# Kernel tuning notes

Hardware: AMD Instinct MI355X
Metric: run time of the kernel (lower is better)

The kernel has to match this reference:

```python
import jax, jax.numpy as jnp
import numpy as np

KROT = 8        # number of pairwise-rotation layers (hard-coded in Rotation)
GROUP = 128     # rotation group size (hard-coded)
QGS = 128       # quantization group size (hard-coded in RotateLinearAWQMarlinInt4)


def setup_inputs() -> dict:
    rng = np.random.default_rng(0)
    M, K, N = 32, 8192, 28672
    G = K // QGS  # 64 quant groups
    shifts = np.arange(8, dtype=np.uint32) * 4
    # activations
    x = jnp.asarray(rng.standard_normal((M, K)), dtype=jnp.float16)
    # int4 weights packed 8-per-int32 along the out dim (nibble j of word n -> column n*8+j)
    nib = rng.integers(0, 16, size=(K, N // 8, 8), dtype=np.uint32)
    qweight = jnp.asarray((nib << shifts).sum(-1, dtype=np.uint32).view(np.int32))  # (K, N//8)
    znib = rng.integers(0, 16, size=(G, N // 8, 8), dtype=np.uint32)
    qzeros = jnp.asarray((znib << shifts).sum(-1, dtype=np.uint32).view(np.int32))  # (G, N//8)
    scales = jnp.asarray(rng.uniform(0.001, 0.01, (G, N)), dtype=jnp.float16)
    bias = jnp.asarray(rng.standard_normal(N) * 0.01, dtype=jnp.float16)
    # rotation params: per-layer angles over all K//2 pairs; one local permutation of
    # 0..127 per layer, shared across all K//GROUP groups (as in Rotation.__init__)
    theta = jnp.asarray(rng.uniform(-0.2, 0.2, (KROT, K // 2)), dtype=jnp.float16)
    pairs = jnp.asarray(np.stack([rng.permutation(GROUP) for _ in range(KROT)]).astype(np.int32))  # (KROT, 128)
    channel_scales = jnp.asarray(rng.uniform(0.5, 2.0, (1, K)), dtype=jnp.float16)
    return dict(x=x, qweight=qweight, qzeros=qzeros, scales=scales, bias=bias,
                theta=theta, pairs=pairs, channel_scales=channel_scales)


def _rotate(x, pairs, theta, channel_scales):
    # x: (M, K). Apply KROT layers of Givens rotations on channel pairs within each
    # 128-wide group, then per-channel scaling.
    M, K = x.shape
    ng = K // GROUP
    xg = x.reshape(M, ng, GROUP)
    for k in range(KROT):
        p = pairs[k]                      # (128,) local permutation
        i, j = p[0::2], p[1::2]           # (64,) disjoint index sets
        th = theta[k].reshape(ng, GROUP // 2).astype(jnp.float32)  # (ng, 64) per-group angles
        c = jnp.cos(th).astype(x.dtype)
        s = jnp.sin(th).astype(x.dtype)
        xi = xg[:, :, i]
        xj = xg[:, :, j]
        xg = xg.at[:, :, i].set(c * xi - s * xj)
        xg = xg.at[:, :, j].set(s * xi + c * xj)
    return xg.reshape(M, K) * channel_scales


def _dequant(qweight, qzeros, scales):
    # unpack 8 uint4 nibbles per int32 along the out dim; dequant per quant group
    K = qweight.shape[0]
    shifts = jnp.arange(8, dtype=jnp.int32) * 4
    w = ((qweight[:, :, None] >> shifts) & 0xF).reshape(K, -1)       # (K, N) ints 0..15
    z = ((qzeros[:, :, None] >> shifts) & 0xF).reshape(qzeros.shape[0], -1)  # (G, N)
    zf = jnp.repeat(z.astype(scales.dtype), QGS, axis=0)             # (K, N)
    sf = jnp.repeat(scales, QGS, axis=0)                             # (K, N)
    return (w.astype(scales.dtype) - zf) * sf


def reference(x, qweight, qzeros, scales, bias, theta, pairs, channel_scales):
    xr = _rotate(x, pairs, theta, channel_scales)   # (M, K)
    W = _dequant(qweight, qzeros, scales)           # (K, N)
    return xr @ W + bias
```

## Files before the change

kernel.cpp:

```cpp
#include <hip/hip_runtime.h>
#include <hip/hip_bf16.h>

using uint32   = unsigned int;
using ushort_t = unsigned short;
using short8   = __attribute__((ext_vector_type(8))) short;
using uint4v   = __attribute__((ext_vector_type(4))) uint32;
using floatx16 = __attribute__((ext_vector_type(16))) float;

#define M_DIM 32
#define K_DIM 8192
#define N_DIM 28672
#define QROW  (N_DIM/8)
#define KSPLIT 8
#define BN    256
#define CH    128
#define NCH   8
#define TSTRIDE 132

typedef __attribute__((address_space(3))) uint32 lds_u32;
typedef const __attribute__((address_space(1))) uint32 glb_u32;

__device__ ushort_t g_xr2[M_DIM * K_DIM];
__device__ float    g_S[64 * M_DIM];

__device__ __forceinline__ float bf2f(ushort_t u){
  unsigned int v = ((unsigned int)u) << 16;
  return __builtin_bit_cast(float, v);
}
__device__ __forceinline__ ushort_t f2bf(float f){
  return __builtin_bit_cast(ushort_t, __float2bfloat16(f));
}

__global__ __launch_bounds__(256) void rotate_kernel(
    const float* __restrict__ x, const float* __restrict__ theta,
    const int* __restrict__ pairs, const float* __restrict__ cs)
{
  __shared__ float xb[4][128];
  const int u    = threadIdx.x >> 6;
  const int lane = threadIdx.x & 63;
  const int id   = blockIdx.x * 4 + u;
  const int m    = id >> 6;
  const int g    = id & 63;
  const float* xp = x + m*K_DIM + g*128;
  int   ip[8], jp[8];
  float cv[8], sv[8];
  #pragma unroll
  for (int k = 0; k < 8; ++k){
    ip[k] = pairs[k*128 + 2*lane];
    jp[k] = pairs[k*128 + 2*lane + 1];
    const float th = theta[k*(K_DIM/2) + g*64 + lane];
    cv[k] = cosf(th); sv[k] = sinf(th);
  }
  xb[u][lane]    = xp[lane];
  xb[u][lane+64] = xp[lane+64];
  #pragma unroll
  for (int k = 0; k < 8; ++k){
    __syncthreads();
    const float xi = xb[u][ip[k]], xj = xb[u][jp[k]];
    xb[u][ip[k]] = cv[k]*xi - sv[k]*xj;
    xb[u][jp[k]] = sv[k]*xi + cv[k]*xj;
  }
  __syncthreads();
  const int base = g*128;
  const int k0 = base + lane, k1 = base + lane + 64;
  const ushort_t b0 = f2bf(xb[u][lane]    * cs[k0]);
  const ushort_t b1 = f2bf(xb[u][lane+64] * cs[k1]);
  g_xr2[(((size_t)(k0>>3))*32 + m)*8 + (k0&7)] = b0;
  g_xr2[(((size_t)(k1>>3))*32 + m)*8 + (k1&7)] = b1;
  float sum = bf2f(b0) + bf2f(b1);
  #pragma unroll
  for (int d = 32; d > 0; d >>= 1) sum += __shfl_xor(sum, d, 64);
  if (lane == 0) g_S[g*M_DIM + m] = sum;
}

__global__ __launch_bounds__(256) void init2_kernel(
    const uint32* __restrict__ qz, const float* __restrict__ scales,
    const float* __restrict__ bias, float* __restrict__ out)
{
  const int n = blockIdx.x*256 + threadIdx.x;
  const uint32 sh = (uint32)((n & 7)*4);
  float acc[M_DIM];
  const float b = bias[n];
  #pragma unroll
  for (int m = 0; m < M_DIM; ++m) acc[m] = b;
  #pragma unroll 1
  for (int g = 0; g < 64; ++g){
    const float s  = scales[(size_t)g*N_DIM + n];
    const uint32 zq = qz[(size_t)g*QROW + (n>>3)];
    const float t  = s * (float)(128u + ((zq >> sh) & 15u));
    #pragma unroll
    for (int m = 0; m < M_DIM; ++m)
      acc[m] = fmaf(-t, g_S[g*M_DIM + m], acc[m]);
  }
  #pragma unroll
  for (int m = 0; m < M_DIM; ++m) out[(size_t)m*N_DIM + n] = acc[m];
}

__global__ __launch_bounds__(512, 4) void gemm_kernel(
    const uint32* __restrict__ qw, const float* __restrict__ scales,
    float* __restrict__ out)
{
  __shared__ uint32   T[32*TSTRIDE];
  __shared__ ushort_t A[2][CH*32];
  const int bid  = blockIdx.x;
  const int ks   = bid & 7;
  const int nb   = bid >> 3;
  const int tid  = threadIdx.x;
  const int w    = tid >> 6;
  const int lane = tid & 63;
  const int l31  = lane & 31;
  const int koct = lane >> 5;
  const int n0   = nb * BN;
  const int n    = n0 + w*32 + l31;
  const uint32 sh = (uint32)((l31 & 7)*4);
  const int col  = w*4 + (l31 >> 3);
  const int k0   = ks * (NCH*CH);

  const int brow = tid >> 3;
  const int bcq  = tid & 7;
  const uint32* bbase = qw + (size_t)(k0 + brow)*QROW + (n0>>3) + bcq*4;
  const ushort_t* abase = g_xr2 + (size_t)k0*32;

  float accT[16];
  #pragma unroll
  for (int r = 0; r < 16; ++r) accT[r] = 0.f;

  uint4v bv[2][2];

  auto stageA = [&](int c){
    const ushort_t* gp = abase + (size_t)c*CH*32 + w*512 + lane*8;
    ushort_t* lp = &A[c & 1][0] + w*512;
    __builtin_amdgcn_global_load_lds((glb_u32*)gp, (lds_u32*)lp, 16, 0, 0);
  };

  bv[0][0] = *(const uint4v*)(bbase);
  bv[0][1] = *(const uint4v*)(bbase + (size_t)64*QROW);
  stageA(0);
  #pragma unroll
  for (int j = 0; j < 4; ++j){
    T[(bcq*4 + j)*TSTRIDE + brow]      = bv[0][0][j];
    T[(bcq*4 + j)*TSTRIDE + brow + 64] = bv[0][1][j];
  }

  #pragma unroll
  for (int c = 0; c < NCH; ++c){
    __syncthreads();
    const int cb = c & 1, nx = cb ^ 1;
    if (c + 1 < NCH){
      const uint32* bb = bbase + (size_t)(c+1)*CH*QROW;
      bv[nx][0] = *(const uint4v*)(bb);
      bv[nx][1] = *(const uint4v*)(bb + (size_t)64*QROW);
      stageA(c+1);
    }
    const float s = scales[(size_t)(ks*NCH + c)*N_DIM + n];
    floatx16 acc;
    #pragma unroll
    for (int r = 0; r < 16; ++r) acc[r] = 0.f;
    #pragma unroll
    for (int kk = 0; kk < 8; ++kk){
      const short8 a = *(const short8*)(&A[cb][((kk*2 + koct)*32 + l31)*8]);
      const uint32* tp = &T[col*TSTRIDE + kk*16 + koct*8];
      const uint4v p0 = *(const uint4v*)(tp);
      const uint4v p1 = *(const uint4v*)(tp + 4);
      uint4v bp;
      bp.x = ((p0.x >> sh) & 15u) | (((p0.y >> sh) & 15u) << 16) | 0x43004300u;
      bp.y = ((p0.z >> sh) & 15u) | (((p0.w >> sh) & 15u) << 16) | 0x43004300u;
      bp.z = ((p1.x >> sh) & 15u) | (((p1.y >> sh) & 15u) << 16) | 0x43004300u;
      bp.w = ((p1.z >> sh) & 15u) | (((p1.w >> sh) & 15u) << 16) | 0x43004300u;
      acc = __builtin_amdgcn_mfma_f32_32x32x16_bf16(
                a, __builtin_bit_cast(short8, bp), acc, 0, 0, 0);
    }
    #pragma unroll
    for (int r = 0; r < 16; ++r) accT[r] = fmaf(s, acc[r], accT[r]);
    __syncthreads();
    if (c + 1 < NCH){
      #pragma unroll
      for (int j = 0; j < 4; ++j){
        T[(bcq*4 + j)*TSTRIDE + brow]      = bv[nx][0][j];
        T[(bcq*4 + j)*TSTRIDE + brow + 64] = bv[nx][1][j];
      }
    }
  }
  #pragma unroll
  for (int r = 0; r < 16; ++r){
    const int row = (r & 3) + 8*(r >> 2) + 4*koct;
    atomicAdd(out + (size_t)row*N_DIM + n, accT[r]);
  }
}

extern "C" void kernel_launch(void* const* d_in, const int* in_sizes, int n_in,
                              void* d_out, int out_size, void* d_ws, size_t ws_size,
                              hipStream_t stream)
{
  const float*  x      = (const float*)d_in[0];
  const uint32* qw     = (const uint32*)d_in[1];
  const uint32* qz     = (const uint32*)d_in[2];
  const float*  scales = (const float*)d_in[3];
  const float*  bias   = (const float*)d_in[4];
  const float*  theta  = (const float*)d_in[5];
  const int*    pairs  = (const int*)d_in[6];
  const float*  cs     = (const float*)d_in[7];
  float* out = (float*)d_out;

  rotate_kernel<<<dim3((M_DIM*64)/4), dim3(256), 0, stream>>>(x, theta, pairs, cs);
  init2_kernel<<<dim3(N_DIM/256), dim3(256), 0, stream>>>(qz, scales, bias, out);
  gemm_kernel<<<dim3((N_DIM/BN)*KSPLIT), dim3(512), 0, stream>>>(qw, scales, out);
}
```

Baseline: 247.7 us.

## Per-wave register nibble transpose and direct global A loads in GEMM

Reworks the int4 GEMM so each wave loads its own 32-column strip of packed weights into registers and does a bit-level 8x8 nibble transpose with shift/xor/mask steps. Each result word then holds 8 consecutive-k nibbles for one column and is stored to a small per-wave double-buffered LDS tile. This removes block-wide __syncthreads and the shared A staging, since activations are read directly from global memory (likely L2-resident). Block size drops to 256 threads with BN=128, doubling the grid. Global weight loads become scalar 4-byte loads and activation reads are repeated per wave, which may raise memory traffic.

```diff
diff --git a/kernel.cpp b/kernel.cpp
--- a/kernel.cpp
+++ b/kernel.cpp
@@ -12,13 +12,9 @@
 #define N_DIM 28672
 #define QROW  (N_DIM/8)
 #define KSPLIT 8
-#define BN    256
+#define BN    128
 #define CH    128
 #define NCH   8
-#define TSTRIDE 132
-
-typedef __attribute__((address_space(3))) uint32 lds_u32;
-typedef const __attribute__((address_space(1))) uint32 glb_u32;
 
 __device__ ushort_t g_xr2[M_DIM * K_DIM];
 __device__ float    g_S[64 * M_DIM];
@@ -96,90 +92,92 @@
   for (int m = 0; m < M_DIM; ++m) out[(size_t)m*N_DIM + n] = acc[m];
 }
 
-__global__ __launch_bounds__(512, 4) void gemm_kernel(
+__global__ __launch_bounds__(256, 4) void gemm_kernel(
     const uint32* __restrict__ qw, const float* __restrict__ scales,
     float* __restrict__ out)
 {
-  __shared__ uint32   T[32*TSTRIDE];
-  __shared__ ushort_t A[2][CH*32];
+  __shared__ uint32 T2[4][2][32*17];
   const int bid  = blockIdx.x;
   const int ks   = bid & 7;
   const int nb   = bid >> 3;
-  const int tid  = threadIdx.x;
-  const int w    = tid >> 6;
-  const int lane = tid & 63;
+  const int w    = (threadIdx.x) >> 6;
+  const int lane = threadIdx.x & 63;
   const int l31  = lane & 31;
   const int koct = lane >> 5;
   const int n0   = nb * BN;
   const int n    = n0 + w*32 + l31;
-  const uint32 sh = (uint32)((l31 & 7)*4);
-  const int col  = w*4 + (l31 >> 3);
   const int k0   = ks * (NCH*CH);
 
-  const int brow = tid >> 3;
-  const int bcq  = tid & 7;
-  const uint32* bbase = qw + (size_t)(k0 + brow)*QROW + (n0>>3) + bcq*4;
-  const ushort_t* abase = g_xr2 + (size_t)k0*32;
+  const int bl_col = lane & 3;
+  const int bl_rb  = (lane >> 2) * 8;
+  const int cw0    = (n0 + w*32) >> 3;
+  const uint32* bbase = qw + (size_t)(k0 + bl_rb)*QROW + cw0 + bl_col;
+  const int wr_koct = (lane >> 2) & 1;
+  const int wr_kk   = lane >> 3;
+  uint32* Tw = &T2[w][0][0];
+
+  const int base_o = k0 >> 3;
 
   float accT[16];
   #pragma unroll
   for (int r = 0; r < 16; ++r) accT[r] = 0.f;
 
-  uint4v bv[2][2];
-
-  auto stageA = [&](int c){
-    const ushort_t* gp = abase + (size_t)c*CH*32 + w*512 + lane*8;
-    ushort_t* lp = &A[c & 1][0] + w*512;
-    __builtin_amdgcn_global_load_lds((glb_u32*)gp, (lds_u32*)lp, 16, 0, 0);
+  uint32 d[8];
+
+  auto loadB = [&](int c){
+    const uint32* bp = bbase + (size_t)c*CH*QROW;
+    #pragma unroll
+    for (int i = 0; i < 8; ++i) d[i] = bp[(size_t)i*QROW];
   };
-
-  bv[0][0] = *(const uint4v*)(bbase);
-  bv[0][1] = *(const uint4v*)(bbase + (size_t)64*QROW);
-  stageA(0);
-  #pragma unroll
-  for (int j = 0; j < 4; ++j){
-    T[(bcq*4 + j)*TSTRIDE + brow]      = bv[0][0][j];
-    T[(bcq*4 + j)*TSTRIDE + brow + 64] = bv[0][1][j];
-  }
-
-  #pragma unroll
+  auto transposeWrite = [&](int c){
+    #pragma unroll
+    for (int s = 0; s < 3; ++s){
+      const int st = 1 << s, sh4 = 4 << s;
+      const uint32 M = (s==0) ? 0x0F0F0F0Fu : (s==1) ? 0x00FF00FFu : 0x0000FFFFu;
+      #pragma unroll
+      for (int i = 0; i < 8; ++i){
+        if (i & st) continue;
+        const uint32 t = ((d[i] >> sh4) ^ d[i+st]) & M;
+        d[i]    ^= t << sh4;
+        d[i+st] ^= t;
+      }
+    }
+    uint32* tb = Tw + (c & 1)*(32*17);
+    #pragma unroll
+    for (int j = 0; j < 8; ++j)
+      tb[(bl_col*8 + j)*17 + wr_koct*8 + wr_kk] = d[j];
+  };
+
+  loadB(0);
+  transposeWrite(0);
+
+  #pragma unroll 1
   for (int c = 0; c < NCH; ++c){
-    __syncthreads();
-    const int cb = c & 1, nx = cb ^ 1;
-    if (c + 1 < NCH){
-      const uint32* bb = bbase + (size_t)(c+1)*CH*QROW;
-      bv[nx][0] = *(const uint4v*)(bb);
-      bv[nx][1] = *(const uint4v*)(bb + (size_t)64*QROW);
-      stageA(c+1);
-    }
+    const uint32* tb = Tw + (c & 1)*(32*17) + l31*17 + koct*8;
+    const uint4v rd0 = *(const uint4v*)(tb);
+    const uint4v rd1 = *(const uint4v*)(tb + 4);
+    if (c + 1 < NCH) loadB(c + 1);
     const float s = scales[(size_t)(ks*NCH + c)*N_DIM + n];
+
     floatx16 acc;
     #pragma unroll
     for (int r = 0; r < 16; ++r) acc[r] = 0.f;
     #pragma unroll
     for (int kk = 0; kk < 8; ++kk){
-      const short8 a = *(const short8*)(&A[cb][((kk*2 + koct)*32 + l31)*8]);
-      const uint32* tp = &T[col*TSTRIDE + kk*16 + koct*8];
-      const uint4v p0 = *(const uint4v*)(tp);
-      const uint4v p1 = *(const uint4v*)(tp + 4);
+      const int o = base_o + c*16 + kk*2 + koct;
+      const short8 a = *(const short8*)(g_xr2 + (size_t)o*256 + l31*8);
+      const uint32 q = (kk < 4) ? rd0[kk] : rd1[kk - 4];
       uint4v bp;
-      bp.x = ((p0.x >> sh) & 15u) | (((p0.y >> sh) & 15u) << 16) | 0x43004300u;
-      bp.y = ((p0.z >> sh) & 15u) | (((p0.w >> sh) & 15u) << 16) | 0x43004300u;
-      bp.z = ((p1.x >> sh) & 15u) | (((p1.y >> sh) & 15u) << 16) | 0x43004300u;
-      bp.w = ((p1.z >> sh) & 15u) | (((p1.w >> sh) & 15u) << 16) | 0x43004300u;
+      bp.x = ( q        & 15u) | (((q >>  4) & 15u) << 16) | 0x43004300u;
+      bp.y = ((q >>  8) & 15u) | (((q >> 12) & 15u) << 16) | 0x43004300u;
+      bp.z = ((q >> 16) & 15u) | (((q >> 20) & 15u) << 16) | 0x43004300u;
+      bp.w = ((q >> 24) & 15u) | ( (q >> 28)        << 16) | 0x43004300u;
       acc = __builtin_amdgcn_mfma_f32_32x32x16_bf16(
                 a, __builtin_bit_cast(short8, bp), acc, 0, 0, 0);
     }
     #pragma unroll
     for (int r = 0; r < 16; ++r) accT[r] = fmaf(s, acc[r], accT[r]);
-    __syncthreads();
-    if (c + 1 < NCH){
-      #pragma unroll
-      for (int j = 0; j < 4; ++j){
-        T[(bcq*4 + j)*TSTRIDE + brow]      = bv[nx][0][j];
-        T[(bcq*4 + j)*TSTRIDE + brow + 64] = bv[nx][1][j];
-      }
-    }
+    if (c + 1 < NCH) transposeWrite(c + 1);
   }
   #pragma unroll
   for (int r = 0; r < 16; ++r){
@@ -204,5 +202,5 @@
 
   rotate_kernel<<<dim3((M_DIM*64)/4), dim3(256), 0, stream>>>(x, theta, pairs, cs);
   init2_kernel<<<dim3(N_DIM/256), dim3(256), 0, stream>>>(qz, scales, bias, out);
-  gemm_kernel<<<dim3((N_DIM/BN)*KSPLIT), dim3(512), 0, stream>>>(qw, scales, out);
-}
+  gemm_kernel<<<dim3((N_DIM/BN)*KSPLIT), dim3(256), 0, stream>>>(qw, scales, out);
+}
```

After: 263.6 us. +6.4%, slower.
